# Kernel optimization log

Measured on AMD Instinct MI355X. Metric: run time of the kernel, lower is better.

## Reference

```python
import jax, jax.numpy as jnp
import numpy as np

N_NODES = 50000
N_EDGES = 800000
N_GRAPHS = 256
F_IN = 256
H_DIM = 64


def setup_inputs() -> dict:
    key = jax.random.key(0)
    ks = jax.random.split(key, 9)
    x = jax.random.normal(ks[0], (N_NODES, F_IN), dtype=jnp.float32)
    edge_index = jax.random.randint(ks[1], (2, N_EDGES), 0, N_NODES, dtype=jnp.int64)
    batch = jnp.sort(jax.random.randint(ks[2], (N_NODES,), 0, N_GRAPHS, dtype=jnp.int64))
    s = 1.0 / np.sqrt(F_IN)
    Wq = jax.random.normal(ks[3], (F_IN, H_DIM), dtype=jnp.float32) * s
    bq = jnp.zeros((H_DIM,), dtype=jnp.float32)
    Wk = jax.random.normal(ks[4], (F_IN, H_DIM), dtype=jnp.float32) * s
    bk = jnp.zeros((H_DIM,), dtype=jnp.float32)
    Wv = jax.random.normal(ks[5], (F_IN, H_DIM), dtype=jnp.float32) * s
    bv = jnp.zeros((H_DIM,), dtype=jnp.float32)
    return {"x": x, "Wq": Wq, "bq": bq, "Wk": Wk, "bk": bk, "Wv": Wv, "bv": bv,
            "edge_index": edge_index, "batch": batch}


def reference(x, Wq, bq, Wk, bk, Wv, bv, edge_index, batch):
    src, dest = edge_index[0], edge_index[1]
    # node projections then per-edge gathers
    q = (x @ Wq + bq)[dest]            # [E, h]
    k = (x @ Wk + bk)[src]             # [E, h]
    v = (x @ Wv + bv)[src]             # [E, h]
    # per-edge dot-product score (bmm of [E,1,h] x [E,h,1])
    prod = jnp.sum(k * q, axis=-1, keepdims=True) / np.sqrt(H_DIM)  # [E, 1]
    exp = jnp.exp(prod)
    seg = batch[src]                   # per-graph segment of source node
    denom = jax.ops.segment_sum(exp, seg, num_segments=N_GRAPHS)    # [G, 1]
    a = exp / (denom[seg] + 1e-6)      # [E, 1]
    out = jax.ops.segment_sum(v * a, dest, num_segments=N_NODES)    # [N, h]
    return out
```

## Files before the change

### kernel.cpp

```cpp
#include <hip/hip_runtime.h>

#define H    64
#define F    256
#define NSEG 256
#define SCB  2048
#define MB   64
#define KC   64
#define XPAD 72
#define NSPAN_MAX 8192

typedef float          f32x4v __attribute__((ext_vector_type(4)));
typedef short          bf16x8 __attribute__((ext_vector_type(8)));
typedef unsigned short u16x4  __attribute__((ext_vector_type(4)));

__global__ __launch_bounds__(1024) void hist8_kernel(
    const int* __restrict__ ei, int* __restrict__ counts8,
    int N, int E, int nspan)
{
    __shared__ int lh[NSPAN_MAX];
    const int p  = blockIdx.x & 7;
    const int c  = blockIdx.x >> 3;
    const int lo = p * nspan;
    const int span = min(N - lo, nspan);
    const int t = threadIdx.x;

    for (int i = t; i < span; i += 1024) lh[i] = 0;
    __syncthreads();

    const int epc = (E + 7) >> 3;
    const int e0 = c * epc;
    const int e1 = min(E, e0 + epc);

    if (((E + e0) & 3) == 0) {
        const int nv = (e1 - e0) >> 2;
        for (int i = t; i < nv; i += 1024) {
            const int4 d4 = *(const int4*)(ei + E + e0 + i * 4);
            int d;
            d = min(max(d4.x, 0), N - 1) - lo; if ((unsigned)d < (unsigned)span) atomicAdd(&lh[d], 1);
            d = min(max(d4.y, 0), N - 1) - lo; if ((unsigned)d < (unsigned)span) atomicAdd(&lh[d], 1);
            d = min(max(d4.z, 0), N - 1) - lo; if ((unsigned)d < (unsigned)span) atomicAdd(&lh[d], 1);
            d = min(max(d4.w, 0), N - 1) - lo; if ((unsigned)d < (unsigned)span) atomicAdd(&lh[d], 1);
        }
        for (int e = e0 + nv * 4 + t; e < e1; e += 1024) {
            const int d = min(max(ei[E + e], 0), N - 1) - lo;
            if ((unsigned)d < (unsigned)span) atomicAdd(&lh[d], 1);
        }
    } else {
        for (int e = e0 + t; e < e1; e += 1024) {
            const int d = min(max(ei[E + e], 0), N - 1) - lo;
            if ((unsigned)d < (unsigned)span) atomicAdd(&lh[d], 1);
        }
    }
    __syncthreads();

    for (int i = t; i < span; i += 1024) counts8[(size_t)c * N + lo + i] = lh[i];
}

#define CVT_WRITE(buf, rr, cc, val) do {                                      \
    const float ff_[4] = {(val).x, (val).y, (val).z, (val).w};                \
    u16x4 h_, l_;                                                             \
    _Pragma("unroll")                                                         \
    for (int u_ = 0; u_ < 4; ++u_) {                                          \
        unsigned ub_ = __float_as_uint(ff_[u_]);                              \
        h_[u_] = (unsigned short)(ub_ >> 16);                                 \
        float rf_ = ff_[u_] - __uint_as_float(ub_ & 0xFFFF0000u);             \
        l_[u_] = (unsigned short)(__float_as_uint(rf_) >> 16);                \
    }                                                                         \
    *(u16x4*)&xs_hi[buf][(rr) * XPAD + (cc) * 4] = h_;                        \
    *(u16x4*)&xs_lo[buf][(rr) * XPAD + (cc) * 4] = l_;                        \
} while (0)

__global__ __launch_bounds__(768, 3) void qkv_mfma(
    const float* __restrict__ x,
    const float* __restrict__ Wq, const float* __restrict__ Wk,
    const float* __restrict__ Wv,
    const float* __restrict__ bq, const float* __restrict__ bk,
    const float* __restrict__ bv,
    float* __restrict__ q, float* __restrict__ k, float* __restrict__ v,
    int N, int ntiles)
{
    __shared__ unsigned short xs_hi[2][MB * XPAD];
    __shared__ unsigned short xs_lo[2][MB * XPAD];

    const int t    = threadIdx.x;
    const int lane = t & 63;
    const int w    = t >> 6;
    const int mat  = w >> 2;
    const int ct   = w & 3;
    const int l15  = lane & 15;
    const int quad = lane >> 4;

    const float* Wm   = (mat == 0) ? Wq : (mat == 1) ? Wk : Wv;
    const float* bias = (mat == 0) ? bq : (mat == 1) ? bk : bv;
    float*       dst  = (mat == 0) ? q  : (mat == 1) ? k  : v;
    const int col = ct * 16 + l15;
    const float bb = bias[col];

    bf16x8 Bh[8], Bl[8];
    #pragma unroll
    for (int u = 0; u < 8; ++u) {
        #pragma unroll
        for (int j = 0; j < 8; ++j) {
            const float f = Wm[(size_t)(u * 32 + quad * 8 + j) * H + col];
            const unsigned ub = __float_as_uint(f);
            Bh[u][j] = (short)(ub >> 16);
            const float rf = f - __uint_as_float(ub & 0xFFFF0000u);
            Bl[u][j] = (short)(__float_as_uint(rf) >> 16);
        }
    }

    const int r0 = t >> 4;
    const int c0 = t & 15;
    const int r1 = (t + 768) >> 4;

    #pragma unroll 1
    for (int tile = blockIdx.x; tile < ntiles; tile += gridDim.x) {
        const int block0 = tile * MB;

        f32x4v acc[4];
        #pragma unroll
        for (int i = 0; i < 4; ++i) acc[i] = (f32x4v)0.f;

        float4 pv0, pv1;
        pv0 = *(const float4*)(x + (size_t)min(block0 + r0, N - 1) * F + c0 * 4);
        if (t < 256)
            pv1 = *(const float4*)(x + (size_t)min(block0 + r1, N - 1) * F + c0 * 4);
        CVT_WRITE(0, r0, c0, pv0);
        if (t < 256) CVT_WRITE(0, r1, c0, pv1);

        #pragma unroll
        for (int c = 0; c < 4; ++c) {
            __syncthreads();

            if (c < 3) {
                const int kb = (c + 1) * KC;
                pv0 = *(const float4*)(x + (size_t)min(block0 + r0, N - 1) * F + kb + c0 * 4);
                if (t < 256)
                    pv1 = *(const float4*)(x + (size_t)min(block0 + r1, N - 1) * F + kb + c0 * 4);
            }

            #pragma unroll
            for (int sk = 0; sk < 2; ++sk) {
                const int u = c * 2 + sk;
                #pragma unroll
                for (int mt = 0; mt < 4; ++mt) {
                    const int ao = (mt * 16 + l15) * XPAD + sk * 32 + quad * 8;
                    const bf16x8 ah = *(const bf16x8*)&xs_hi[c & 1][ao];
                    const bf16x8 al = *(const bf16x8*)&xs_lo[c & 1][ao];
                    f32x4v a = acc[mt];
                    a = __builtin_amdgcn_mfma_f32_16x16x32_bf16(ah, Bh[u], a, 0, 0, 0);
                    a = __builtin_amdgcn_mfma_f32_16x16x32_bf16(ah, Bl[u], a, 0, 0, 0);
                    a = __builtin_amdgcn_mfma_f32_16x16x32_bf16(al, Bh[u], a, 0, 0, 0);
                    acc[mt] = a;
                }
            }

            if (c < 3) {
                const int nb = (c & 1) ^ 1;
                CVT_WRITE(nb, r0, c0, pv0);
                if (t < 256) CVT_WRITE(nb, r1, c0, pv1);
            }
        }

        #pragma unroll
        for (int mt = 0; mt < 4; ++mt) {
            #pragma unroll
            for (int r = 0; r < 4; ++r) {
                const int node = block0 + mt * 16 + quad * 4 + r;
                if (node < N)
                    dst[(size_t)node * H + col] = acc[mt][r] + bb;
            }
        }
    }
}

__global__ __launch_bounds__(256) void scanA(
    const int* __restrict__ counts8, int* __restrict__ counts,
    int* __restrict__ offsets, int* __restrict__ bsum, int n)
{
    __shared__ int ps[256];
    const int t = threadIdx.x;
    const int i0 = blockIdx.x * SCB + t * 8;
    int loc[8];
    int s = 0;
    #pragma unroll
    for (int u = 0; u < 8; ++u) {
        int i = i0 + u;
        int c = 0;
        if (i < n) {
            #pragma unroll
            for (int p = 0; p < 8; ++p) c += counts8[(size_t)p * n + i];
            counts[i] = c;
            c = (c + 3) & ~3;
        }
        loc[u] = s; s += c;
    }
    ps[t] = s;
    __syncthreads();
    for (int off = 1; off < 256; off <<= 1) {
        int a = (t >= off) ? ps[t - off] : 0;
        __syncthreads();
        ps[t] += a;
        __syncthreads();
    }
    const int base = ps[t] - s;
    #pragma unroll
    for (int u = 0; u < 8; ++u) {
        int i = i0 + u;
        if (i < n) offsets[i] = base + loc[u];
    }
    if (t == 255) bsum[blockIdx.x] = ps[255];
}

__global__ void scanB(int* __restrict__ bsum, int nb)
{
    const int t = threadIdx.x;
    int v = (t < nb) ? bsum[t] : 0;
    int inc = v;
    #pragma unroll
    for (int off = 1; off < 64; off <<= 1) {
        int u = __shfl_up(inc, off, 64);
        if (t >= off) inc += u;
    }
    if (t < nb) bsum[t] = inc - v;
}

__global__ __launch_bounds__(256) void scanC(
    const int* __restrict__ bsum, int* __restrict__ offsets,
    int* __restrict__ cursor, int n)
{
    const int i0 = blockIdx.x * SCB + threadIdx.x * 8;
    const int add = bsum[blockIdx.x];
    #pragma unroll
    for (int u = 0; u < 8; ++u) {
        int i = i0 + u;
        if (i < n) { int o = offsets[i] + add; offsets[i] = o; cursor[i] = o; }
    }
}

__global__ __launch_bounds__(256) void reorder_kernel(
    const int* __restrict__ ei, const int* __restrict__ batch,
    int* __restrict__ cursor, unsigned* __restrict__ epack,
    int E, int N, int nspan)
{
    const int p  = blockIdx.x & 7;
    const int ci = blockIdx.x >> 3;
    const int lo = p * nspan;
    const int hi = min(N, lo + nspan);
    const int e0 = ci * 1024 + threadIdx.x * 4;

    int d[4];
    if (e0 + 3 < E) {
        const int4 d4 = *(const int4*)(ei + E + e0);
        d[0] = d4.x; d[1] = d4.y; d[2] = d4.z; d[3] = d4.w;
    } else {
        #pragma unroll
        for (int u = 0; u < 4; ++u)
            d[u] = (e0 + u < E) ? ei[E + e0 + u] : -1;
    }

    #pragma unroll
    for (int u = 0; u < 4; ++u) {
        const int dst = min(max(d[u], 0), N - 1);
        if (d[u] >= 0 && dst >= lo && dst < hi) {
            int src = ei[e0 + u];
            src = min(max(src, 0), N - 1);
            int seg = batch[src];
            seg = min(max(seg, 0), NSEG - 1);
            const int pos = atomicAdd(&cursor[dst], 1);
            epack[pos] = (unsigned)src | ((unsigned)seg << 16);
        }
    }
}

__global__ __launch_bounds__(256) void score_kernel(
    const float* __restrict__ q, const float* __restrict__ k,
    const unsigned* __restrict__ epack,
    const int* __restrict__ offsets, const int* __restrict__ counts,
    float* __restrict__ exps, float* __restrict__ denom8, int N)
{
    __shared__ float sden[NSEG];
    const int t = threadIdx.x;
    sden[t] = 0.f;
    __syncthreads();

    const int lane16 = t & 15;
    const int grp    = (t >> 4) & 3;
    const int wave   = t >> 6;
    const int nwaves = gridDim.x * 4;

    const float4* q4 = (const float4*)q;
    const float4* k4 = (const float4*)k;

    for (int n = blockIdx.x * 4 + wave; n < N; n += nwaves) {
        const int off = offsets[n];
        const int cnt = counts[n];
        if (cnt == 0) continue;
        const float4 qv = q4[(size_t)n * 16 + lane16];
        for (int i = grp; i < cnt; i += 4) {
            const int pos = off + i;
            const unsigned p = epack[pos];
            const int src = p & 0xFFFF;
            const float4 kv = k4[(size_t)src * 16 + lane16];
            float d = kv.x * qv.x + kv.y * qv.y + kv.z * qv.z + kv.w * qv.w;
            d += __shfl_xor(d, 1, 64);
            d += __shfl_xor(d, 2, 64);
            d += __shfl_xor(d, 4, 64);
            d += __shfl_xor(d, 8, 64);
            if (lane16 == 0) {
                float ex = __expf(d * 0.125f);
                exps[pos] = ex;
                atomicAdd(&sden[(p >> 16) & 255], ex);
            }
        }
    }
    __syncthreads();
    float ds = sden[t];
    if (ds != 0.f) atomicAdd(&denom8[(blockIdx.x & 7) * NSEG + t], ds);
}

__global__ __launch_bounds__(256) void accum_kernel(
    const float* __restrict__ v, const float* __restrict__ exps,
    const unsigned* __restrict__ epack,
    const int* __restrict__ offsets, const int* __restrict__ counts,
    const float* __restrict__ denom8, float* __restrict__ out, int N)
{
    __shared__ float rden[NSEG];
    const int t = threadIdx.x;
    {
        float dsum = 0.f;
        #pragma unroll
        for (int p = 0; p < 8; ++p) dsum += denom8[p * NSEG + t];
        rden[t] = 1.0f / (dsum + 1e-6f);
    }
    __syncthreads();

    const int lane = t & 63;
    const int wave = t >> 6;
    const int n = blockIdx.x * 4 + wave;
    if (n >= N) return;

    const int off = offsets[n];
    const int cnt = counts[n];

    float acc = 0.f;
    int i = 0;
    for (; i + 8 <= cnt; i += 8) {
        const uint4  pa = *(const uint4*)(epack + off + i);
        const uint4  pb = *(const uint4*)(epack + off + i + 4);
        const float4 ea = *(const float4*)(exps + off + i);
        const float4 eb = *(const float4*)(exps + off + i + 4);
        const float v0 = v[(size_t)(pa.x & 0xFFFF) * H + lane];
        const float v1 = v[(size_t)(pa.y & 0xFFFF) * H + lane];
        const float v2 = v[(size_t)(pa.z & 0xFFFF) * H + lane];
        const float v3 = v[(size_t)(pa.w & 0xFFFF) * H + lane];
        const float v4_ = v[(size_t)(pb.x & 0xFFFF) * H + lane];
        const float v5 = v[(size_t)(pb.y & 0xFFFF) * H + lane];
        const float v6 = v[(size_t)(pb.z & 0xFFFF) * H + lane];
        const float v7 = v[(size_t)(pb.w & 0xFFFF) * H + lane];
        acc = fmaf(v0, ea.x * rden[(pa.x >> 16) & 255], acc);
        acc = fmaf(v1, ea.y * rden[(pa.y >> 16) & 255], acc);
        acc = fmaf(v2, ea.z * rden[(pa.z >> 16) & 255], acc);
        acc = fmaf(v3, ea.w * rden[(pa.w >> 16) & 255], acc);
        acc = fmaf(v4_, eb.x * rden[(pb.x >> 16) & 255], acc);
        acc = fmaf(v5, eb.y * rden[(pb.y >> 16) & 255], acc);
        acc = fmaf(v6, eb.z * rden[(pb.z >> 16) & 255], acc);
        acc = fmaf(v7, eb.w * rden[(pb.w >> 16) & 255], acc);
    }
    for (; i + 4 <= cnt; i += 4) {
        const uint4  pp = *(const uint4*)(epack + off + i);
        const float4 ee = *(const float4*)(exps + off + i);
        const float v0 = v[(size_t)(pp.x & 0xFFFF) * H + lane];
        const float v1 = v[(size_t)(pp.y & 0xFFFF) * H + lane];
        const float v2 = v[(size_t)(pp.z & 0xFFFF) * H + lane];
        const float v3 = v[(size_t)(pp.w & 0xFFFF) * H + lane];
        acc = fmaf(v0, ee.x * rden[(pp.x >> 16) & 255], acc);
        acc = fmaf(v1, ee.y * rden[(pp.y >> 16) & 255], acc);
        acc = fmaf(v2, ee.z * rden[(pp.z >> 16) & 255], acc);
        acc = fmaf(v3, ee.w * rden[(pp.w >> 16) & 255], acc);
    }
    for (; i < cnt; ++i) {
        const unsigned p = epack[off + i];
        acc = fmaf(v[(size_t)(p & 0xFFFF) * H + lane],
                   exps[off + i] * rden[(p >> 16) & 255], acc);
    }
    out[(size_t)n * H + lane] = acc;
}

extern "C" void kernel_launch(void* const* d_in, const int* in_sizes, int n_in,
                              void* d_out, int out_size, void* d_ws, size_t ws_size,
                              hipStream_t stream)
{
    const float* x   = (const float*)d_in[0];
    const float* Wq  = (const float*)d_in[1];
    const float* bq  = (const float*)d_in[2];
    const float* Wk  = (const float*)d_in[3];
    const float* bk  = (const float*)d_in[4];
    const float* Wv  = (const float*)d_in[5];
    const float* bv  = (const float*)d_in[6];
    const int* ei    = (const int*)d_in[7];
    const int* batch = (const int*)d_in[8];

    const int N = in_sizes[8];
    const int E = in_sizes[7] / 2;
    const int EP = E + 3 * N + 16;

    float*    q       = (float*)d_ws;
    float*    k       = q + (size_t)N * H;
    float*    v       = k + (size_t)N * H;
    float*    exps    = v + (size_t)N * H;
    unsigned* epack   = (unsigned*)(exps + EP);
    int*      counts  = (int*)(epack + EP);
    int*      offsets = counts + N;
    int*      cursor  = offsets + N;
    int*      bsum    = cursor + N;
    float*    denom8  = (float*)(bsum + 64);
    int*      counts8 = (int*)(denom8 + 8 * NSEG);

    hipMemsetAsync(denom8, 0, 8 * NSEG * sizeof(float), stream);

    const int NT    = (N + MB - 1) / MB;
    const int NC    = (E + 1023) / 1024;
    const int nspan = (N + 7) / 8;
    const int NBSC  = (N + SCB - 1) / SCB;

    hist8_kernel<<<64, 1024, 0, stream>>>(ei, counts8, N, E, nspan);

    qkv_mfma<<<256, 768, 0, stream>>>(
        x, Wq, Wk, Wv, bq, bk, bv, q, k, v, N, NT);

    scanA<<<NBSC, 256, 0, stream>>>(counts8, counts, offsets, bsum, N);
    scanB<<<1, 64, 0, stream>>>(bsum, NBSC);
    scanC<<<NBSC, 256, 0, stream>>>(bsum, offsets, cursor, N);

    reorder_kernel<<<8 * NC, 256, 0, stream>>>(
        ei, batch, cursor, epack, E, N, nspan);

    score_kernel<<<2048, 256, 0, stream>>>(
        q, k, epack, offsets, counts, exps, denom8, N);

    accum_kernel<<<(N + 3) / 4, 256, 0, stream>>>(
        v, exps, epack, offsets, counts, denom8, (float*)d_out, N);
}
```

Before: 267.9 us.

## Route reorder work by XCD via work queues and swizzle QKV shared memory

The reorder kernel becomes a persistent grid. Each block reads its hardware XCC ID and first pulls edge chunks from a work queue for the destination-node range matching its XCD, then moves on to the other ranges. The aim is to keep the cursor atomics and epack scatter for each range inside one XCD's L2. The score kernel's denominator partials are indexed by XCC ID, and the QKV shared-memory tiles switch from row padding to an XOR swizzle to avoid LDS bank conflicts while using less LDS. The risks are queue-atomic overhead, the per-chunk syncthreads, and reliance on hardware-register semantics.

```diff
diff --git a/kernel.cpp b/kernel.cpp
--- a/kernel.cpp
+++ b/kernel.cpp
@@ -6,12 +6,18 @@
 #define SCB  2048
 #define MB   64
 #define KC   64
-#define XPAD 72
 #define NSPAN_MAX 8192
+#define RCH  4096
 
 typedef float          f32x4v __attribute__((ext_vector_type(4)));
 typedef short          bf16x8 __attribute__((ext_vector_type(8)));
 typedef unsigned short u16x4  __attribute__((ext_vector_type(4)));
+
+__device__ __forceinline__ int xcc_id() {
+    int x;
+    asm volatile("s_getreg_b32 %0, hwreg(HW_REG_XCC_ID)" : "=s"(x));
+    return x & 7;
+}
 
 __global__ __launch_bounds__(1024) void hist8_kernel(
     const int* __restrict__ ei, int* __restrict__ counts8,
@@ -66,8 +72,10 @@
         float rf_ = ff_[u_] - __uint_as_float(ub_ & 0xFFFF0000u);             \
         l_[u_] = (unsigned short)(__float_as_uint(rf_) >> 16);                \
     }                                                                         \
-    *(u16x4*)&xs_hi[buf][(rr) * XPAD + (cc) * 4] = h_;                        \
-    *(u16x4*)&xs_lo[buf][(rr) * XPAD + (cc) * 4] = l_;                        \
+    const int so_ = (rr) * 64 + (((((cc) >> 1) ^ ((rr) & 7))) << 3)           \
+                  + ((cc) & 1) * 4;                                           \
+    *(u16x4*)&xs_hi[buf][so_] = h_;                                           \
+    *(u16x4*)&xs_lo[buf][so_] = l_;                                           \
 } while (0)
 
 __global__ __launch_bounds__(768, 3) void qkv_mfma(
@@ -79,8 +87,8 @@
     float* __restrict__ q, float* __restrict__ k, float* __restrict__ v,
     int N, int ntiles)
 {
-    __shared__ unsigned short xs_hi[2][MB * XPAD];
-    __shared__ unsigned short xs_lo[2][MB * XPAD];
+    __shared__ unsigned short xs_hi[2][MB * 64];
+    __shared__ unsigned short xs_lo[2][MB * 64];
 
     const int t    = threadIdx.x;
     const int lane = t & 63;
@@ -113,6 +121,8 @@
     const int c0 = t & 15;
     const int r1 = (t + 768) >> 4;
 
+    const int swz = (l15 & 7);
+
     #pragma unroll 1
     for (int tile = blockIdx.x; tile < ntiles; tile += gridDim.x) {
         const int block0 = tile * MB;
@@ -144,7 +154,8 @@
                 const int u = c * 2 + sk;
                 #pragma unroll
                 for (int mt = 0; mt < 4; ++mt) {
-                    const int ao = (mt * 16 + l15) * XPAD + sk * 32 + quad * 8;
+                    const int row = mt * 16 + l15;
+                    const int ao  = row * 64 + (((sk * 4 + quad) ^ swz) << 3);
                     const bf16x8 ah = *(const bf16x8*)&xs_hi[c & 1][ao];
                     const bf16x8 al = *(const bf16x8*)&xs_lo[c & 1][ao];
                     f32x4v a = acc[mt];
@@ -241,34 +252,54 @@
 __global__ __launch_bounds__(256) void reorder_kernel(
     const int* __restrict__ ei, const int* __restrict__ batch,
     int* __restrict__ cursor, unsigned* __restrict__ epack,
-    int E, int N, int nspan)
-{
-    const int p  = blockIdx.x & 7;
-    const int ci = blockIdx.x >> 3;
-    const int lo = p * nspan;
-    const int hi = min(N, lo + nspan);
-    const int e0 = ci * 1024 + threadIdx.x * 4;
-
-    int d[4];
-    if (e0 + 3 < E) {
-        const int4 d4 = *(const int4*)(ei + E + e0);
-        d[0] = d4.x; d[1] = d4.y; d[2] = d4.z; d[3] = d4.w;
-    } else {
-        #pragma unroll
-        for (int u = 0; u < 4; ++u)
-            d[u] = (e0 + u < E) ? ei[E + e0 + u] : -1;
-    }
-
-    #pragma unroll
-    for (int u = 0; u < 4; ++u) {
-        const int dst = min(max(d[u], 0), N - 1);
-        if (d[u] >= 0 && dst >= lo && dst < hi) {
-            int src = ei[e0 + u];
-            src = min(max(src, 0), N - 1);
-            int seg = batch[src];
-            seg = min(max(seg, 0), NSEG - 1);
-            const int pos = atomicAdd(&cursor[dst], 1);
-            epack[pos] = (unsigned)src | ((unsigned)seg << 16);
+    int* __restrict__ wq, int E, int N, int nspan, int nchunk)
+{
+    __shared__ int chunk_s;
+    const int t   = threadIdx.x;
+    const int xcd = xcc_id();
+
+    for (int cc = 0; cc < 8; ++cc) {
+        const int cls = (xcd + cc) & 7;
+        const int lo  = cls * nspan;
+        const int hi  = min(N, lo + nspan);
+        for (;;) {
+            __syncthreads();
+            if (t == 0) chunk_s = atomicAdd(&wq[cls], 1);
+            __syncthreads();
+            const int ci = chunk_s;
+            if (ci >= nchunk) break;
+            const int base = ci * RCH;
+            #pragma unroll
+            for (int it = 0; it < 4; ++it) {
+                const int e0 = base + it * 1024 + t * 4;
+                if (e0 + 3 < E) {
+                    const int4 d4 = *(const int4*)(ei + E + e0);
+                    const int dd[4] = {d4.x, d4.y, d4.z, d4.w};
+                    #pragma unroll
+                    for (int u = 0; u < 4; ++u) {
+                        const int dst = min(max(dd[u], 0), N - 1);
+                        if (dst >= lo && dst < hi) {
+                            const int src = min(max(ei[e0 + u], 0), N - 1);
+                            const int seg = min(max(batch[src], 0), NSEG - 1);
+                            const int pos = atomicAdd(&cursor[dst], 1);
+                            epack[pos] = (unsigned)src | ((unsigned)seg << 16);
+                        }
+                    }
+                } else {
+                    for (int u = 0; u < 4; ++u) {
+                        const int e = e0 + u;
+                        if (e < E) {
+                            const int dst = min(max(ei[E + e], 0), N - 1);
+                            if (dst >= lo && dst < hi) {
+                                const int src = min(max(ei[e], 0), N - 1);
+                                const int seg = min(max(batch[src], 0), NSEG - 1);
+                                const int pos = atomicAdd(&cursor[dst], 1);
+                                epack[pos] = (unsigned)src | ((unsigned)seg << 16);
+                            }
+                        }
+                    }
+                }
+            }
         }
     }
 }
@@ -316,7 +347,7 @@
     }
     __syncthreads();
     float ds = sden[t];
-    if (ds != 0.f) atomicAdd(&denom8[(blockIdx.x & 7) * NSEG + t], ds);
+    if (ds != 0.f) atomicAdd(&denom8[xcc_id() * NSEG + t], ds);
 }
 
 __global__ __launch_bounds__(256) void accum_kernel(
@@ -415,13 +446,14 @@
     int*      cursor  = offsets + N;
     int*      bsum    = cursor + N;
     float*    denom8  = (float*)(bsum + 64);
-    int*      counts8 = (int*)(denom8 + 8 * NSEG);
-
-    hipMemsetAsync(denom8, 0, 8 * NSEG * sizeof(float), stream);
+    int*      wq      = (int*)(denom8 + 8 * NSEG);
+    int*      counts8 = wq + 16;
+
+    hipMemsetAsync(denom8, 0, 8 * NSEG * sizeof(float) + 16 * sizeof(int), stream);
 
     const int NT    = (N + MB - 1) / MB;
-    const int NC    = (E + 1023) / 1024;
     const int nspan = (N + 7) / 8;
+    const int NRCH  = (E + RCH - 1) / RCH;
     const int NBSC  = (N + SCB - 1) / SCB;
 
     hist8_kernel<<<64, 1024, 0, stream>>>(ei, counts8, N, E, nspan);
@@ -433,8 +465,8 @@
     scanB<<<1, 64, 0, stream>>>(bsum, NBSC);
     scanC<<<NBSC, 256, 0, stream>>>(bsum, offsets, cursor, N);
 
-    reorder_kernel<<<8 * NC, 256, 0, stream>>>(
-        ei, batch, cursor, epack, E, N, nspan);
+    reorder_kernel<<<2048, 256, 0, stream>>>(
+        ei, batch, cursor, epack, wq, E, N, nspan, NRCH);
 
     score_kernel<<<2048, 256, 0, stream>>>(
         q, k, epack, offsets, counts, exps, denom8, N);
```

Measured after the change: 451.2 us. 68.4% more time.
